# Performance work log

Hardware: AMD Instinct MI355X
Metric: run time of the kernel (lower is better)

## Reference

```python
import jax, jax.numpy as jnp
import numpy as np

EMBED = 1024
HEADS = 16
HEAD_DIM = EMBED // HEADS
LN_EPS = 1e-5
XNORM_GAMMA = 0.01


def xnorm(x, gamma):
    # x * gamma / ||x||_4 along last dim (keepdim)
    norm4 = jnp.sum(x ** 4, axis=-1, keepdims=True) ** 0.25
    return x * gamma / norm4


def setup_inputs() -> dict:
    key = jax.random.key(0)
    ks = jax.random.split(key, 12)
    B, S = 2, 2048
    sc_hd = 1.0 / np.sqrt(HEAD_DIM)
    sc_e = 1.0 / np.sqrt(EMBED)
    return {
        "value": jax.random.normal(ks[0], (B, S, EMBED), jnp.float32),
        "key": jax.random.normal(ks[1], (B, S, EMBED), jnp.float32),
        "query": jax.random.normal(ks[2], (B, S, EMBED), jnp.float32),
        # per-head projections, torch Linear convention: y = x @ W.T
        "Wq": jax.random.normal(ks[3], (HEAD_DIM, HEAD_DIM), jnp.float32) * sc_hd,
        "Wk": jax.random.normal(ks[4], (HEAD_DIM, HEAD_DIM), jnp.float32) * sc_hd,
        "Wv": jax.random.normal(ks[5], (HEAD_DIM, HEAD_DIM), jnp.float32) * sc_hd,
        "Wo": jax.random.normal(ks[6], (EMBED, EMBED), jnp.float32) * sc_e,
        "bo": jnp.zeros((EMBED,), jnp.float32),
        "ln_w": jnp.ones((EMBED,), jnp.float32),
        "ln_b": jnp.zeros((EMBED,), jnp.float32),
        "Wsq": jax.random.normal(ks[7], (EMBED, EMBED), jnp.float32) * sc_e,
        "bsq": jnp.zeros((EMBED,), jnp.float32),
    }


def reference(value, key, query, Wq, Wk, Wv, Wo, bo, ln_w, ln_b, Wsq, bsq):
    B, S, E = query.shape
    # split heads: [B, S, H, D]
    v = value.reshape(B, S, HEADS, HEAD_DIM)
    k = key.reshape(B, S, HEADS, HEAD_DIM)
    q = query.reshape(B, S, HEADS, HEAD_DIM)
    v = jnp.einsum('nshd,ed->nshe', v, Wv)
    k = jnp.einsum('nshd,ed->nshe', k, Wk)
    q = jnp.einsum('nshd,ed->nshe', q, Wq)
    # energy: [B, H, Sq, Sk]
    energy = jnp.einsum('nqhd,nkhd->nhqk', q, k)
    energy_n = xnorm(energy, XNORM_GAMMA)
    v_n = xnorm(v, XNORM_GAMMA)
    out = jnp.einsum('nhql,nlhd->nqhd', energy_n, v_n).reshape(B, S, E)
    attn = out @ Wo.T + bo
    # LayerNorm(attention + query) over embed dim
    x = attn + query
    mu = jnp.mean(x, axis=-1, keepdims=True)
    var = jnp.mean((x - mu) ** 2, axis=-1, keepdims=True)
    x = (x - mu) / jnp.sqrt(var + LN_EPS) * ln_w + ln_b
    # SE gating: x * sigmoid(Linear(x))
    gate = jax.nn.sigmoid(x @ Wsq.T + bsq)
    return x * gate
```

## Files before the change

### kernel.cpp

```cpp
#include <hip/hip_runtime.h>
#include <stdint.h>

#define B_ 2
#define S_ 2048
#define E_ 1024
#define H_ 16
#define HD_ 64
#define N_ (B_*S_)
#define BH_ (B_*H_)
#define GAMMA 0.01f

typedef __attribute__((ext_vector_type(8))) short bf16x8;
typedef __attribute__((ext_vector_type(4))) float f32x4;
typedef __attribute__((ext_vector_type(2))) float f32x2;
typedef __attribute__((ext_vector_type(16))) float f32x16;
typedef __attribute__((ext_vector_type(4))) unsigned int u32x4;
typedef unsigned short u16;
typedef unsigned int u32;

#define SWZ(row, kb) ((kb) ^ (((row)&7)<<4))

__device__ __forceinline__ u16 f2bf(float f){
  union { float f; u32 u; } v; v.f = f;
  return (u16)((v.u + 0x7FFFu + ((v.u>>16)&1u)) >> 16);
}

__device__ __forceinline__ float bf2f(u16 u){
  union { u32 u; float f; } v; v.u = ((u32)u)<<16; return v.f;
}

__device__ __forceinline__ u32 cvt_pk_bf16(float lo, float hi){
  u32 r; asm("v_cvt_pk_bf16_f32 %0, %1, %2" : "=v"(r) : "v"(lo), "v"(hi)); return r;
}

__device__ __forceinline__ uint4 pack8(float4 a, float4 b){
  uint4 r;
  r.x = cvt_pk_bf16(a.x, a.y);
  r.y = cvt_pk_bf16(a.z, a.w);
  r.z = cvt_pk_bf16(b.x, b.y);
  r.w = cvt_pk_bf16(b.z, b.w);
  return r;
}

__device__ __forceinline__ bf16x8 ldfrag(const unsigned char* base, int row, int kbyte){
  return *reinterpret_cast<const bf16x8*>(base + row*128 + SWZ(row, kbyte));
}
__device__ __forceinline__ bf16x8 ldfragV(const unsigned char* base, int row, int col){
  return *reinterpret_cast<const bf16x8*>(base + row*256 + (col ^ ((row&15)<<4)));
}

__device__ __forceinline__ void gl_lds16(const void* g, void* l){
  __builtin_amdgcn_global_load_lds(
      (const __attribute__((address_space(1))) unsigned int*)g,
      (__attribute__((address_space(3))) unsigned int*)l, 16, 0, 0);
}

__device__ __forceinline__ void proj_mfma(const unsigned char* X, const unsigned char* W,
                                          int wid, int l15, int g4, f32x4 acc[4])
{
  f32x4 z = {0.f,0.f,0.f,0.f};
  acc[0]=z; acc[1]=z; acc[2]=z; acc[3]=z;
  #pragma unroll
  for (int kk=0;kk<2;++kk){
    int kbyte = kk*64 + g4*16;
    bf16x8 a = ldfrag(X, wid*16 + l15, kbyte);
    #pragma unroll
    for (int t=0;t<4;++t){
      bf16x8 w = ldfrag(W, t*16 + l15, kbyte);
      acc[t] = __builtin_amdgcn_mfma_f32_16x16x32_bf16(a, w, acc[t], 0, 0, 0);
    }
  }
}

__global__ __launch_bounds__(256) void k_proj(
    const float* __restrict__ qin, const float* __restrict__ kin, const float* __restrict__ vin,
    const float* __restrict__ Wq, const float* __restrict__ Wk, const float* __restrict__ Wv,
    u16* __restrict__ qp, u16* __restrict__ kp, u16* __restrict__ vnT,
    const float* __restrict__ Wo, const float* __restrict__ Wsq,
    u16* __restrict__ wo16, u16* __restrict__ wsq16)
{
  __shared__ alignas(16) unsigned char sm[49152];
  if (blockIdx.y >= H_){
    int cblk = (blockIdx.y - H_)*64 + blockIdx.x;
    int n4 = (E_*E_)/4;
    for (int i = cblk*256 + threadIdx.x; i < 2*n4; i += 128*256){
      const float4* src; ushort4* dst; int j;
      if (i < n4){ src=(const float4*)Wo;  dst=(ushort4*)wo16;  j=i; }
      else       { src=(const float4*)Wsq; dst=(ushort4*)wsq16; j=i-n4; }
      float4 v = src[j];
      ushort4 p; p.x=f2bf(v.x); p.y=f2bf(v.y); p.z=f2bf(v.z); p.w=f2bf(v.w);
      dst[j] = p;
    }
    return;
  }
  const int XQ=0, XK=8192, XV=16384, WQS=24576, WKS=32768, WVS=40960;
  int tid = threadIdx.x, lane = tid&63, wid = tid>>6;
  int l15 = lane&15, g4 = lane>>4;
  int tb = blockIdx.x*64;
  int h  = blockIdx.y;
  int b  = tb >> 11;
  int sbase = tb & 2047;
  int bh = b*H_ + h;

  {
    int rl = tid>>2;
    int d0 = (tid&3)*16;
    const float* xs[3] = { qin, kin, vin };
    const float* wsrc[3] = { Wq, Wk, Wv };
    const int xoff[3] = {XQ,XK,XV}, woff[3] = {WQS,WKS,WVS};
    #pragma unroll
    for (int m3=0;m3<3;++m3){
      const float4* gx = reinterpret_cast<const float4*>(xs[m3] + (size_t)(tb+rl)*E_ + h*HD_ + d0);
      float4 a=gx[0], bb=gx[1], c=gx[2], d=gx[3];
      *(uint4*)(sm + xoff[m3] + rl*128 + SWZ(rl, d0*2))    = pack8(a,bb);
      *(uint4*)(sm + xoff[m3] + rl*128 + SWZ(rl, d0*2+16)) = pack8(c,d);
      const float4* gw = reinterpret_cast<const float4*>(wsrc[m3] + rl*64 + d0);
      float4 e=gw[0], f=gw[1], g2=gw[2], h2=gw[3];
      *(uint4*)(sm + woff[m3] + rl*128 + SWZ(rl, d0*2))    = pack8(e,f);
      *(uint4*)(sm + woff[m3] + rl*128 + SWZ(rl, d0*2+16)) = pack8(g2,h2);
    }
  }
  __syncthreads();

  f32x4 qacc[4], kacc[4], vacc[4];
  proj_mfma(sm+XQ, sm+WQS, wid, l15, g4, qacc);
  proj_mfma(sm+XK, sm+WKS, wid, l15, g4, kacc);
  proj_mfma(sm+XV, sm+WVS, wid, l15, g4, vacc);

  {
    float p4r[4] = {0.f,0.f,0.f,0.f};
    #pragma unroll
    for (int t=0;t<4;++t)
      #pragma unroll
      for (int r=0;r<4;++r){ float e = vacc[t][r]; float e2 = e*e; p4r[r] += e2*e2; }
    #pragma unroll
    for (int r=0;r<4;++r){
      float p = p4r[r];
      p += __shfl_xor(p,1); p += __shfl_xor(p,2); p += __shfl_xor(p,4); p += __shfl_xor(p,8);
      p4r[r] = GAMMA / sqrtf(sqrtf(p));
    }
    #pragma unroll
    for (int t=0;t<4;++t)
      #pragma unroll
      for (int r=0;r<4;++r) vacc[t][r] *= p4r[r];
  }

  __syncthreads();

  #pragma unroll
  for (int t=0;t<4;++t){
    int dd = t*16 + l15;
    #pragma unroll
    for (int r=0;r<4;++r){
      int tokl = wid*16 + g4*4 + r;
      *(u16*)(sm + XQ + tokl*128 + SWZ(tokl, dd*2)) = f2bf(qacc[t][r]);
      *(u16*)(sm + XK + tokl*128 + SWZ(tokl, dd*2)) = f2bf(kacc[t][r]);
    }
    #pragma unroll
    for (int r=0;r<4;r+=2){
      int tokl = wid*16 + g4*4 + r;
      *(u32*)(sm + XV + dd*128 + SWZ(dd, tokl*2)) = cvt_pk_bf16(vacc[t][r], vacc[t][r+1]);
    }
  }
  __syncthreads();

  {
    int rl = tid>>2; int c2 = tid&3;
    uint4 q0 = *(const uint4*)(sm + XQ + rl*128 + SWZ(rl, c2*32));
    uint4 q1 = *(const uint4*)(sm + XQ + rl*128 + SWZ(rl, c2*32+16));
    size_t qg = ((size_t)bh*S_ + sbase + rl)*HD_ + c2*16;
    *(uint4*)(qp + qg)     = q0;
    *(uint4*)(qp + qg + 8) = q1;
    uint4 k0 = *(const uint4*)(sm + XK + rl*128 + SWZ(rl, c2*32));
    uint4 k1 = *(const uint4*)(sm + XK + rl*128 + SWZ(rl, c2*32+16));
    *(uint4*)(kp + qg)     = k0;
    *(uint4*)(kp + qg + 8) = k1;
    uint4 v0 = *(const uint4*)(sm + XV + rl*128 + SWZ(rl, c2*32));
    uint4 v1 = *(const uint4*)(sm + XV + rl*128 + SWZ(rl, c2*32+16));
    size_t vg = ((size_t)bh*HD_ + rl)*S_ + sbase + c2*16;
    *(uint4*)(vnT + vg)     = v0;
    *(uint4*)(vnT + vg + 8) = v1;
  }
}

__global__ __launch_bounds__(256, 2) void k_attn(
    const u16* __restrict__ qp, const u16* __restrict__ kp,
    const u16* __restrict__ vnT, u16* __restrict__ ao)
{
  __shared__ alignas(128) unsigned char sm[81920];
  char* smc = (char*)sm;
  int tid = threadIdx.x, lane = tid&63, wv = tid>>6;
  int l31 = lane&31, hi = lane>>5;
  int qi = wv>>1, kj = wv&1;
  int L = blockIdx.x;
  int xcd = L&7, iw = L>>3;
  int bh = xcd*4 + (iw>>4);
  int qx = iw&15;
  int qb = qx*128;
  int b = bh>>4, h = bh&15;
  const u16* Kb = kp  + (size_t)bh*S_*HD_;
  const u16* Vb = vnT + (size_t)bh*HD_*S_;
  const u16* Qb = qp  + (size_t)bh*S_*HD_;
  int q0 = qb + qi*64;

  bf16x8 qf[2][4];
  #pragma unroll
  for (int f=0;f<2;++f)
    #pragma unroll
    for (int kk=0;kk<4;++kk)
      qf[f][kk] = *reinterpret_cast<const bf16x8*>(Qb + (size_t)(q0 + f*32 + l31)*HD_ + kk*16 + hi*8);

  f32x16 z16 = {};
  f32x16 o[2][2];
  #pragma unroll
  for (int f=0;f<2;++f){ o[f][0] = z16; o[f][1] = z16; }
  f32x2 p4a[2] = {{0.f,0.f},{0.f,0.f}};
  f32x2 p4b[2] = {{0.f,0.f},{0.f,0.f}};

  const char* kSrcC[4]; const char* vSrcC[4];
  #pragma unroll
  for (int c=0;c<4;++c){
    int rk = wv*32 + c*8 + (lane>>3);
    int ck = ((lane&7)*16) ^ ((rk&7)<<4);
    kSrcC[c] = (const char*)Kb + (size_t)rk*128 + ck;
    int rv = wv*16 + c*4 + (lane>>4);
    int cv = ((lane&15)*16) ^ ((rv&15)<<4);
    vSrcC[c] = (const char*)Vb + (size_t)rv*4096 + cv;
  }

  auto STAGE_K = [&](int bsel, int kt){
    char* db = smc + bsel*16384 + wv*4096;
    #pragma unroll
    for (int c=0;c<4;++c) gl_lds16(kSrcC[c] + (size_t)kt*16384, db + c*1024);
  };
  auto STAGE_V = [&](int bsel, int kt){
    char* db = smc + 49152 + bsel*16384 + wv*4096;
    #pragma unroll
    for (int c=0;c<4;++c) gl_lds16(vSrcC[c] + (size_t)kt*256, db + c*1024);
  };

  auto PACK = [&](const f32x16& e, u32 (&w)[4][2], f32x2& pa){
    #pragma unroll
    for (int j=0;j<8;++j){
      const int g=j>>1, i=j&1;
      float a = e[4*g+2*i], c = e[4*g+2*i+1];
      f32x2 pr = {a, c};
      f32x2 e2;
      asm("v_pk_mul_f32 %0, %1, %1" : "=v"(e2) : "v"(pr));
      asm("v_pk_fma_f32 %0, %1, %1, %0" : "+v"(pa) : "v"(e2));
      w[g][i] = cvt_pk_bf16(a, c);
    }
  };
  auto AFRAG = [&](u32 (&w)[4][2], int s) -> bf16x8 {
    u32 a0 = w[2*s][0], b0 = w[2*s+1][0];
    u32 a1 = w[2*s][1], b1 = w[2*s+1][1];
    asm("v_permlane32_swap_b32 %0, %1" : "+v"(a0), "+v"(b0));
    asm("v_permlane32_swap_b32 %0, %1" : "+v"(a1), "+v"(b1));
    u32x4 fw = {a0, a1, b0, b1};
    return __builtin_bit_cast(bf16x8, fw);
  };

  auto QK = [&](const unsigned char* K_, int s2, f32x16& E0, f32x16& E1){
    bf16x8 ka[4];
    #pragma unroll
    for (int kk=0;kk<4;++kk) ka[kk] = ldfrag(K_, kj*64 + s2*32 + l31, kk*32 + hi*16);
    E0 = z16; E1 = z16;
    __builtin_amdgcn_s_setprio(1);
    #pragma unroll
    for (int kk=0;kk<4;++kk){
      E0 = __builtin_amdgcn_mfma_f32_32x32x16_bf16(ka[kk], qf[0][kk], E0, 0,0,0);
      E1 = __builtin_amdgcn_mfma_f32_32x32x16_bf16(ka[kk], qf[1][kk], E1, 0,0,0);
    }
    __builtin_amdgcn_s_setprio(0);
  };

  auto PVF = [&](const unsigned char* V_, int s2, u32 (&w0)[4][2], u32 (&w1)[4][2]){
    bf16x8 vb[2][2];
    #pragma unroll
    for (int s=0;s<2;++s){
      vb[s][0] = ldfragV(V_, l31,    kj*128 + s2*64 + s*32 + hi*16);
      vb[s][1] = ldfragV(V_, 32+l31, kj*128 + s2*64 + s*32 + hi*16);
    }
    __builtin_amdgcn_s_setprio(1);
    #pragma unroll
    for (int s=0;s<2;++s){
      bf16x8 ef0 = AFRAG(w0, s);
      bf16x8 ef1 = AFRAG(w1, s);
      o[0][0] = __builtin_amdgcn_mfma_f32_32x32x16_bf16(ef0, vb[s][0], o[0][0], 0,0,0);
      o[0][1] = __builtin_amdgcn_mfma_f32_32x32x16_bf16(ef0, vb[s][1], o[0][1], 0,0,0);
      o[1][0] = __builtin_amdgcn_mfma_f32_32x32x16_bf16(ef1, vb[s][0], o[1][0], 0,0,0);
      o[1][1] = __builtin_amdgcn_mfma_f32_32x32x16_bf16(ef1, vb[s][1], o[1][1], 0,0,0);
    }
    __builtin_amdgcn_s_setprio(0);
  };

  const int NT = S_/128;
  STAGE_K(0, 0); STAGE_V(0, 0); STAGE_K(1, 1);

  f32x16 eA0, eA1, eB0, eB1;
  u32 wA0[4][2], wA1[4][2], wB0[4][2], wB1[4][2];

  #pragma unroll 1
  for (int t=0; t<NT; ++t){
    if (t < NT-1) { asm volatile("s_waitcnt vmcnt(4)" ::: "memory"); }
    else          { asm volatile("s_waitcnt vmcnt(0)" ::: "memory"); }
    __builtin_amdgcn_s_barrier();
    asm volatile("" ::: "memory");
    if (t+1 < NT) STAGE_V((t+1)&1, t+1);
    if (t+2 < NT) STAGE_K((t+2)%3, t+2);

    const unsigned char* K_ = sm + (t%3)*16384;
    const unsigned char* V_ = sm + 49152 + (t&1)*16384;

    QK(K_, 0, eA0, eA1);
    QK(K_, 1, eB0, eB1);
    PACK(eA0, wA0, p4a[0]);
    PACK(eA1, wA1, p4a[1]);
    PVF(V_, 0, wA0, wA1);
    PACK(eB0, wB0, p4b[0]);
    PACK(eB1, wB1, p4b[1]);
    PVF(V_, 1, wB0, wB1);
  }

  float p4f[2];
  #pragma unroll
  for (int f=0;f<2;++f) p4f[f] = p4a[f].x + p4a[f].y + p4b[f].x + p4b[f].y;

  __syncthreads();
  float* red  = (float*)smc;
  float* redp = (float*)(smc + 32768);
  if (kj==1){
    #pragma unroll
    for (int f=0;f<2;++f){
      #pragma unroll
      for (int ds=0;ds<2;++ds){
        float* dst = red + ((((qi*2+f)*2+ds)*64 + lane)*16);
        #pragma unroll
        for (int r4=0;r4<4;++r4)
          *(float4*)(dst + r4*4) = make_float4(o[f][ds][r4*4],o[f][ds][r4*4+1],o[f][ds][r4*4+2],o[f][ds][r4*4+3]);
      }
      redp[(qi*2+f)*64 + lane] = p4f[f];
    }
  }
  __syncthreads();
  if (kj==0){
    #pragma unroll
    for (int f=0;f<2;++f){
      #pragma unroll
      for (int ds=0;ds<2;++ds){
        const float* srcp = red + ((((qi*2+f)*2+ds)*64 + lane)*16);
        #pragma unroll
        for (int r4=0;r4<4;++r4){
          float4 t = *(const float4*)(srcp + r4*4);
          o[f][ds][r4*4]+=t.x; o[f][ds][r4*4+1]+=t.y; o[f][ds][r4*4+2]+=t.z; o[f][ds][r4*4+3]+=t.w;
        }
      }
      p4f[f] += redp[(qi*2+f)*64 + lane];
      p4f[f] += __shfl_xor(p4f[f], 32);
    }
    float sc0 = GAMMA * rsqrtf(sqrtf(p4f[0]));
    float sc1 = GAMMA * rsqrtf(sqrtf(p4f[1]));
    #pragma unroll
    for (int f=0;f<2;++f){
      #pragma unroll
      for (int r=0;r<16;++r){
        int qrow = (r&3) + 8*(r>>2) + 4*hi;
        float scr = __shfl(f==0 ? sc0 : sc1, qrow);
        size_t n = (size_t)b*S_ + q0 + f*32 + qrow;
        u16* dst = ao + n*E_ + h*HD_;
        dst[l31]    = f2bf(o[f][0][r] * scr);
        dst[32+l31] = f2bf(o[f][1][r] * scr);
      }
    }
  }
}

template<int MODE>
__global__ __launch_bounds__(256, 2) void k_gemm(
    const u16* __restrict__ A, const u16* __restrict__ Bw,
    const float* __restrict__ bias, const float* __restrict__ auxf,
    const u16* __restrict__ aux16, float* __restrict__ out32, u16* __restrict__ out16)
{
  __shared__ alignas(128) unsigned char sm[65536];
  char* smc = (char*)sm;
  int tid = threadIdx.x, lane = tid&63, wv = tid>>6;
  int l31 = lane&31, hi = lane>>5;
  int wr = wv>>1, wc = wv&1;
  int LL = (blockIdx.x & 7)*32 + (blockIdx.x >> 3);
  int mt = LL >> 3, nt = LL & 7;
  int m0 = mt*128, n0 = nt*128;

  const char* aS[4]; const char* bS[4];
  #pragma unroll
  for (int c=0;c<4;++c){
    int off = wv*4096 + c*1024 + lane*16;
    int r = off>>7, cl = off&127;
    int cs = cl ^ ((r&7)<<4);
    aS[c] = (const char*)A  + ((size_t)(m0+r)*E_)*2 + cs;
    bS[c] = (const char*)Bw + ((size_t)(n0+r)*E_)*2 + cs;
  }

  auto STAGE = [&](int bsel, int t){
    char* db = smc + bsel*32768 + wv*4096;
    size_t kb2 = (size_t)t*128;
    #pragma unroll
    for (int c=0;c<4;++c) gl_lds16(aS[c] + kb2, db + c*1024);
    #pragma unroll
    for (int c=0;c<4;++c) gl_lds16(bS[c] + kb2, db + 16384 + c*1024);
  };

  f32x16 acc[2][2] = {{{}, {}}, {{}, {}}};

  const int NK = E_/64;
  STAGE(0, 0); STAGE(1, 1);

  #pragma unroll 1
  for (int t=0; t<NK; ++t){
    if (t < NK-1) { asm volatile("s_waitcnt vmcnt(8)" ::: "memory"); }
    else          { asm volatile("s_waitcnt vmcnt(0)" ::: "memory"); }
    __builtin_amdgcn_s_barrier();
    asm volatile("" ::: "memory");

    const unsigned char* Ap_ = sm + (t&1)*32768;
    const unsigned char* Bp_ = Ap_ + 16384;
    #pragma unroll
    for (int kk=0;kk<4;++kk){
      int kbyte = kk*32 + hi*16;
      bf16x8 a0 = ldfrag(Ap_, wr*64 + l31,      kbyte);
      bf16x8 a1 = ldfrag(Ap_, wr*64 + 32 + l31, kbyte);
      bf16x8 b0 = ldfrag(Bp_, wc*64 + l31,      kbyte);
      bf16x8 b1 = ldfrag(Bp_, wc*64 + 32 + l31, kbyte);
      __builtin_amdgcn_s_setprio(1);
      acc[0][0] = __builtin_amdgcn_mfma_f32_32x32x16_bf16(a0, b0, acc[0][0], 0,0,0);
      acc[0][1] = __builtin_amdgcn_mfma_f32_32x32x16_bf16(a0, b1, acc[0][1], 0,0,0);
      acc[1][0] = __builtin_amdgcn_mfma_f32_32x32x16_bf16(a1, b0, acc[1][0], 0,0,0);
      acc[1][1] = __builtin_amdgcn_mfma_f32_32x32x16_bf16(a1, b1, acc[1][1], 0,0,0);
      __builtin_amdgcn_s_setprio(0);
    }

    asm volatile("" ::: "memory");
    __builtin_amdgcn_s_barrier();
    asm volatile("" ::: "memory");
    if (t+2 < NK) STAGE(t&1, t+2);
  }

  #pragma unroll
  for (int cg=0;cg<2;++cg){
    int col = n0 + wc*64 + cg*32 + l31;
    float bi = bias[col];
    #pragma unroll
    for (int rg=0;rg<2;++rg)
      #pragma unroll
      for (int r=0;r<16;++r){
        int mrow = m0 + wr*64 + rg*32 + (r&3) + 8*(r>>2) + 4*hi;
        size_t idx = (size_t)mrow*E_ + col;
        float v = acc[rg][cg][r] + bi;
        if (MODE == 0){
          out16[idx] = f2bf(v + auxf[idx]);
        } else {
          float gg = 1.f/(1.f + __expf(-v));
          out32[idx] = bf2f(aux16[idx]) * gg;
        }
      }
  }
}

__global__ __launch_bounds__(256) void k_ln(
    const u16* __restrict__ xin, const float* __restrict__ lnw, const float* __restrict__ lnb,
    u16* __restrict__ xout)
{
  __shared__ float red[8];
  __shared__ float stats[2];
  int row = blockIdx.x, tid = threadIdx.x;
  ushort4 xr = reinterpret_cast<const ushort4*>(xin + (size_t)row*E_)[tid];
  float x0 = bf2f(xr.x), x1 = bf2f(xr.y), x2 = bf2f(xr.z), x3 = bf2f(xr.w);
  float s  = x0 + x1 + x2 + x3;
  float s2 = x0*x0 + x1*x1 + x2*x2 + x3*x3;
  #pragma unroll
  for (int m=1;m<64;m<<=1){ s += __shfl_xor(s,m); s2 += __shfl_xor(s2,m); }
  if ((tid&63)==0){ red[tid>>6] = s; red[4+(tid>>6)] = s2; }
  __syncthreads();
  if (tid==0){
    float ts  = red[0]+red[1]+red[2]+red[3];
    float ts2 = red[4]+red[5]+red[6]+red[7];
    float mu  = ts * (1.f/E_);
    float var = ts2 * (1.f/E_) - mu*mu;
    stats[0] = mu; stats[1] = rsqrtf(var + 1e-5f);
  }
  __syncthreads();
  float mu = stats[0], rstd = stats[1];
  float4 w  = reinterpret_cast<const float4*>(lnw)[tid];
  float4 bb = reinterpret_cast<const float4*>(lnb)[tid];
  ushort4 p;
  p.x = f2bf((x0-mu)*rstd*w.x + bb.x);
  p.y = f2bf((x1-mu)*rstd*w.y + bb.y);
  p.z = f2bf((x2-mu)*rstd*w.z + bb.z);
  p.w = f2bf((x3-mu)*rstd*w.w + bb.w);
  reinterpret_cast<ushort4*>(xout + (size_t)row*E_)[tid] = p;
}

extern "C" void kernel_launch(void* const* d_in, const int* in_sizes, int n_in,
                              void* d_out, int out_size, void* d_ws, size_t ws_size,
                              hipStream_t stream)
{
  const float* value = (const float*)d_in[0];
  const float* key   = (const float*)d_in[1];
  const float* query = (const float*)d_in[2];
  const float* Wq    = (const float*)d_in[3];
  const float* Wk    = (const float*)d_in[4];
  const float* Wv    = (const float*)d_in[5];
  const float* Wo    = (const float*)d_in[6];
  const float* bo    = (const float*)d_in[7];
  const float* lnw   = (const float*)d_in[8];
  const float* lnb   = (const float*)d_in[9];
  const float* Wsq   = (const float*)d_in[10];
  const float* bsq   = (const float*)d_in[11];
  float* out = (float*)d_out;

  char* ws = (char*)d_ws;
  const size_t MB = 1ull<<20;
  u16*   qp     = (u16*)(ws + 0*MB);
  u16*   kp     = (u16*)(ws + 8*MB);
  u16*   vnT    = (u16*)(ws + 16*MB);
  u16*   ao     = (u16*)(ws + 24*MB);
  u16*   xres16 = (u16*)(ws + 8*MB);
  u16*   x16    = (u16*)(ws + 16*MB);
  u16*   wo16   = (u16*)(ws + 48*MB);
  u16*   wsq16  = (u16*)(ws + 50*MB);

  k_proj<<<dim3(N_/64, H_+2), 256, 0, stream>>>(query, key, value, Wq, Wk, Wv,
                                                qp, kp, vnT, Wo, Wsq, wo16, wsq16);
  k_attn<<<512, 256, 0, stream>>>(qp, kp, vnT, ao);
  k_gemm<0><<<256, 256, 0, stream>>>(ao, wo16, bo, query, (const u16*)nullptr, (float*)nullptr, xres16);
  k_ln  <<<N_, 256, 0, stream>>>(xres16, lnw, lnb, x16);
  k_gemm<1><<<256, 256, 0, stream>>>(x16, wsq16, bsq, (const float*)nullptr, x16, out, (u16*)nullptr);
}
```

Before: 104.5 us.

## Reassociate attention as Q·(KᵀV) with a separate per-head KᵀV kernel

There is no softmax, and the row-wise 4-norm scale of the energy matrix can be applied after the product. The change therefore computes M = Kᵀ·V_n once per head (64x64) in a new kernel and produces each output row as (q·M) scaled by the energy norm. The attention kernel now only needs the energy pass to accumulate sum(e^4) per query row, and it drops the P·V MFMAs, the V staging and the bf16 packing of the energy. The cost is an extra transposed-K write in the projection kernel and an extra small launch, plus a different rounding order.

```diff
diff --git a/kernel.cpp b/kernel.cpp
--- a/kernel.cpp
+++ b/kernel.cpp
@@ -14,7 +14,6 @@
 typedef __attribute__((ext_vector_type(4))) float f32x4;
 typedef __attribute__((ext_vector_type(2))) float f32x2;
 typedef __attribute__((ext_vector_type(16))) float f32x16;
-typedef __attribute__((ext_vector_type(4))) unsigned int u32x4;
 typedef unsigned short u16;
 typedef unsigned int u32;
 
@@ -45,9 +44,6 @@
 __device__ __forceinline__ bf16x8 ldfrag(const unsigned char* base, int row, int kbyte){
   return *reinterpret_cast<const bf16x8*>(base + row*128 + SWZ(row, kbyte));
 }
-__device__ __forceinline__ bf16x8 ldfragV(const unsigned char* base, int row, int col){
-  return *reinterpret_cast<const bf16x8*>(base + row*256 + (col ^ ((row&15)<<4)));
-}
 
 __device__ __forceinline__ void gl_lds16(const void* g, void* l){
   __builtin_amdgcn_global_load_lds(
@@ -75,7 +71,7 @@
 __global__ __launch_bounds__(256) void k_proj(
     const float* __restrict__ qin, const float* __restrict__ kin, const float* __restrict__ vin,
     const float* __restrict__ Wq, const float* __restrict__ Wk, const float* __restrict__ Wv,
-    u16* __restrict__ qp, u16* __restrict__ kp, u16* __restrict__ vnT,
+    u16* __restrict__ qp, u16* __restrict__ kp, u16* __restrict__ kpT, u16* __restrict__ vnT,
     const float* __restrict__ Wo, const float* __restrict__ Wsq,
     u16* __restrict__ wo16, u16* __restrict__ wsq16)
 {
@@ -159,7 +155,8 @@
     #pragma unroll
     for (int r=0;r<4;r+=2){
       int tokl = wid*16 + g4*4 + r;
-      *(u32*)(sm + XV + dd*128 + SWZ(dd, tokl*2)) = cvt_pk_bf16(vacc[t][r], vacc[t][r+1]);
+      *(u32*)(sm + XV  + dd*128 + SWZ(dd, tokl*2)) = cvt_pk_bf16(vacc[t][r], vacc[t][r+1]);
+      *(u32*)(sm + WQS + dd*128 + SWZ(dd, tokl*2)) = cvt_pk_bf16(kacc[t][r], kacc[t][r+1]);
     }
   }
   __syncthreads();
@@ -175,19 +172,111 @@
     uint4 k1 = *(const uint4*)(sm + XK + rl*128 + SWZ(rl, c2*32+16));
     *(uint4*)(kp + qg)     = k0;
     *(uint4*)(kp + qg + 8) = k1;
+    size_t vg = ((size_t)bh*HD_ + rl)*S_ + sbase + c2*16;
     uint4 v0 = *(const uint4*)(sm + XV + rl*128 + SWZ(rl, c2*32));
     uint4 v1 = *(const uint4*)(sm + XV + rl*128 + SWZ(rl, c2*32+16));
-    size_t vg = ((size_t)bh*HD_ + rl)*S_ + sbase + c2*16;
     *(uint4*)(vnT + vg)     = v0;
     *(uint4*)(vnT + vg + 8) = v1;
+    uint4 t0 = *(const uint4*)(sm + WQS + rl*128 + SWZ(rl, c2*32));
+    uint4 t1 = *(const uint4*)(sm + WQS + rl*128 + SWZ(rl, c2*32+16));
+    *(uint4*)(kpT + vg)     = t0;
+    *(uint4*)(kpT + vg + 8) = t1;
+  }
+}
+
+__global__ __launch_bounds__(256) void k_kv(
+    const u16* __restrict__ kpT, const u16* __restrict__ vnT, u16* __restrict__ MT)
+{
+  __shared__ alignas(128) unsigned char sm[32768];
+  char* smc = (char*)sm;
+  int tid = threadIdx.x, lane = tid&63, wv = tid>>6;
+  int l31 = lane&31, hi = lane>>5;
+  int bh = blockIdx.x;
+  const u16* kt = kpT + (size_t)bh*HD_*S_;
+  const u16* vt = vnT + (size_t)bh*HD_*S_;
+
+  f32x16 acc[2][2] = {{{}, {}}, {{}, {}}};
+  int sbase = wv*512 + hi*8;
+
+  #pragma unroll 2
+  for (int it=0; it<32; ++it){
+    int so = sbase + it*16;
+    bf16x8 ka0 = *reinterpret_cast<const bf16x8*>(kt + (size_t)l31*S_      + so);
+    bf16x8 ka1 = *reinterpret_cast<const bf16x8*>(kt + (size_t)(32+l31)*S_ + so);
+    bf16x8 vb0 = *reinterpret_cast<const bf16x8*>(vt + (size_t)l31*S_      + so);
+    bf16x8 vb1 = *reinterpret_cast<const bf16x8*>(vt + (size_t)(32+l31)*S_ + so);
+    acc[0][0] = __builtin_amdgcn_mfma_f32_32x32x16_bf16(ka0, vb0, acc[0][0], 0,0,0);
+    acc[0][1] = __builtin_amdgcn_mfma_f32_32x32x16_bf16(ka1, vb0, acc[0][1], 0,0,0);
+    acc[1][0] = __builtin_amdgcn_mfma_f32_32x32x16_bf16(ka0, vb1, acc[1][0], 0,0,0);
+    acc[1][1] = __builtin_amdgcn_mfma_f32_32x32x16_bf16(ka1, vb1, acc[1][1], 0,0,0);
+  }
+
+  auto wrAcc = [&](int sl){
+    float* base = (float*)(smc + sl*16384);
+    #pragma unroll
+    for (int eh=0;eh<2;++eh)
+      #pragma unroll
+      for (int dh=0;dh<2;++dh){
+        float* dst = base + (((eh*2+dh)*64 + lane)*16);
+        #pragma unroll
+        for (int r4=0;r4<4;++r4)
+          *(float4*)(dst + r4*4) = make_float4(acc[eh][dh][r4*4],acc[eh][dh][r4*4+1],
+                                               acc[eh][dh][r4*4+2],acc[eh][dh][r4*4+3]);
+      }
+  };
+  auto addAcc = [&](int sl){
+    const float* base = (const float*)(smc + sl*16384);
+    #pragma unroll
+    for (int eh=0;eh<2;++eh)
+      #pragma unroll
+      for (int dh=0;dh<2;++dh){
+        const float* srcp = base + (((eh*2+dh)*64 + lane)*16);
+        #pragma unroll
+        for (int r4=0;r4<4;++r4){
+          float4 t = *(const float4*)(srcp + r4*4);
+          acc[eh][dh][r4*4]+=t.x; acc[eh][dh][r4*4+1]+=t.y;
+          acc[eh][dh][r4*4+2]+=t.z; acc[eh][dh][r4*4+3]+=t.w;
+        }
+      }
+  };
+
+  if (wv==1) wrAcc(0);
+  if (wv==3) wrAcc(1);
+  __syncthreads();
+  if (wv==0) addAcc(0);
+  if (wv==2) addAcc(1);
+  __syncthreads();
+  if (wv==2) wrAcc(0);
+  __syncthreads();
+  if (wv==0) addAcc(0);
+  __syncthreads();
+  if (wv==0){
+    #pragma unroll
+    for (int eh=0;eh<2;++eh)
+      #pragma unroll
+      for (int dh=0;dh<2;++dh)
+        #pragma unroll
+        for (int r=0;r<16;r+=2){
+          int e = eh*32 + l31;
+          int d = dh*32 + (r&3) + 8*(r>>2) + 4*hi;
+          *(u32*)(smc + e*128 + SWZ(e, d*2)) = cvt_pk_bf16(acc[eh][dh][r], acc[eh][dh][r+1]);
+        }
+  }
+  __syncthreads();
+  if (wv==0){
+    u16* dst = MT + (size_t)bh*4096 + lane*64;
+    #pragma unroll
+    for (int c=0;c<8;++c)
+      *(uint4*)(dst + c*8) = *(const uint4*)(smc + lane*128 + SWZ(lane, c*16));
   }
 }
 
 __global__ __launch_bounds__(256, 2) void k_attn(
     const u16* __restrict__ qp, const u16* __restrict__ kp,
-    const u16* __restrict__ vnT, u16* __restrict__ ao)
-{
-  __shared__ alignas(128) unsigned char sm[81920];
+    const u16* __restrict__ MT, u16* __restrict__ ao)
+{
+  __shared__ alignas(128) unsigned char sm[49152];
+  __shared__ float px[256];
   char* smc = (char*)sm;
   int tid = threadIdx.x, lane = tid&63, wv = tid>>6;
   int l31 = lane&31, hi = lane>>5;
@@ -198,9 +287,8 @@
   int qx = iw&15;
   int qb = qx*128;
   int b = bh>>4, h = bh&15;
-  const u16* Kb = kp  + (size_t)bh*S_*HD_;
-  const u16* Vb = vnT + (size_t)bh*HD_*S_;
-  const u16* Qb = qp  + (size_t)bh*S_*HD_;
+  const u16* Kb = kp + (size_t)bh*S_*HD_;
+  const u16* Qb = qp + (size_t)bh*S_*HD_;
   int q0 = qb + qi*64;
 
   bf16x8 qf[2][4];
@@ -211,21 +299,15 @@
       qf[f][kk] = *reinterpret_cast<const bf16x8*>(Qb + (size_t)(q0 + f*32 + l31)*HD_ + kk*16 + hi*8);
 
   f32x16 z16 = {};
-  f32x16 o[2][2];
-  #pragma unroll
-  for (int f=0;f<2;++f){ o[f][0] = z16; o[f][1] = z16; }
   f32x2 p4a[2] = {{0.f,0.f},{0.f,0.f}};
   f32x2 p4b[2] = {{0.f,0.f},{0.f,0.f}};
 
-  const char* kSrcC[4]; const char* vSrcC[4];
+  const char* kSrcC[4];
   #pragma unroll
   for (int c=0;c<4;++c){
     int rk = wv*32 + c*8 + (lane>>3);
     int ck = ((lane&7)*16) ^ ((rk&7)<<4);
     kSrcC[c] = (const char*)Kb + (size_t)rk*128 + ck;
-    int rv = wv*16 + c*4 + (lane>>4);
-    int cv = ((lane&15)*16) ^ ((rv&15)<<4);
-    vSrcC[c] = (const char*)Vb + (size_t)rv*4096 + cv;
   }
 
   auto STAGE_K = [&](int bsel, int kt){
@@ -233,31 +315,15 @@
     #pragma unroll
     for (int c=0;c<4;++c) gl_lds16(kSrcC[c] + (size_t)kt*16384, db + c*1024);
   };
-  auto STAGE_V = [&](int bsel, int kt){
-    char* db = smc + 49152 + bsel*16384 + wv*4096;
-    #pragma unroll
-    for (int c=0;c<4;++c) gl_lds16(vSrcC[c] + (size_t)kt*256, db + c*1024);
-  };
-
-  auto PACK = [&](const f32x16& e, u32 (&w)[4][2], f32x2& pa){
+
+  auto P4ACC = [&](const f32x16& e, f32x2& pa){
     #pragma unroll
     for (int j=0;j<8;++j){
-      const int g=j>>1, i=j&1;
-      float a = e[4*g+2*i], c = e[4*g+2*i+1];
-      f32x2 pr = {a, c};
+      f32x2 pr = {e[2*j], e[2*j+1]};
       f32x2 e2;
       asm("v_pk_mul_f32 %0, %1, %1" : "=v"(e2) : "v"(pr));
       asm("v_pk_fma_f32 %0, %1, %1, %0" : "+v"(pa) : "v"(e2));
-      w[g][i] = cvt_pk_bf16(a, c);
-    }
-  };
-  auto AFRAG = [&](u32 (&w)[4][2], int s) -> bf16x8 {
-    u32 a0 = w[2*s][0], b0 = w[2*s+1][0];
-    u32 a1 = w[2*s][1], b1 = w[2*s+1][1];
-    asm("v_permlane32_swap_b32 %0, %1" : "+v"(a0), "+v"(b0));
-    asm("v_permlane32_swap_b32 %0, %1" : "+v"(a1), "+v"(b1));
-    u32x4 fw = {a0, a1, b0, b1};
-    return __builtin_bit_cast(bf16x8, fw);
+    }
   };
 
   auto QK = [&](const unsigned char* K_, int s2, f32x16& E0, f32x16& E1){
@@ -274,31 +340,10 @@
     __builtin_amdgcn_s_setprio(0);
   };
 
-  auto PVF = [&](const unsigned char* V_, int s2, u32 (&w0)[4][2], u32 (&w1)[4][2]){
-    bf16x8 vb[2][2];
-    #pragma unroll
-    for (int s=0;s<2;++s){
-      vb[s][0] = ldfragV(V_, l31,    kj*128 + s2*64 + s*32 + hi*16);
-      vb[s][1] = ldfragV(V_, 32+l31, kj*128 + s2*64 + s*32 + hi*16);
-    }
-    __builtin_amdgcn_s_setprio(1);
-    #pragma unroll
-    for (int s=0;s<2;++s){
-      bf16x8 ef0 = AFRAG(w0, s);
-      bf16x8 ef1 = AFRAG(w1, s);
-      o[0][0] = __builtin_amdgcn_mfma_f32_32x32x16_bf16(ef0, vb[s][0], o[0][0], 0,0,0);
-      o[0][1] = __builtin_amdgcn_mfma_f32_32x32x16_bf16(ef0, vb[s][1], o[0][1], 0,0,0);
-      o[1][0] = __builtin_amdgcn_mfma_f32_32x32x16_bf16(ef1, vb[s][0], o[1][0], 0,0,0);
-      o[1][1] = __builtin_amdgcn_mfma_f32_32x32x16_bf16(ef1, vb[s][1], o[1][1], 0,0,0);
-    }
-    __builtin_amdgcn_s_setprio(0);
-  };
-
   const int NT = S_/128;
-  STAGE_K(0, 0); STAGE_V(0, 0); STAGE_K(1, 1);
+  STAGE_K(0, 0); STAGE_K(1, 1);
 
   f32x16 eA0, eA1, eB0, eB1;
-  u32 wA0[4][2], wA1[4][2], wB0[4][2], wB1[4][2];
 
   #pragma unroll 1
   for (int t=0; t<NT; ++t){
@@ -306,72 +351,62 @@
     else          { asm volatile("s_waitcnt vmcnt(0)" ::: "memory"); }
     __builtin_amdgcn_s_barrier();
     asm volatile("" ::: "memory");
-    if (t+1 < NT) STAGE_V((t+1)&1, t+1);
     if (t+2 < NT) STAGE_K((t+2)%3, t+2);
 
     const unsigned char* K_ = sm + (t%3)*16384;
-    const unsigned char* V_ = sm + 49152 + (t&1)*16384;
-
     QK(K_, 0, eA0, eA1);
     QK(K_, 1, eB0, eB1);
-    PACK(eA0, wA0, p4a[0]);
-    PACK(eA1, wA1, p4a[1]);
-    PVF(V_, 0, wA0, wA1);
-    PACK(eB0, wB0, p4b[0]);
-    PACK(eB1, wB1, p4b[1]);
-    PVF(V_, 1, wB0, wB1);
+    P4ACC(eA0, p4a[0]);
+    P4ACC(eA1, p4a[1]);
+    P4ACC(eB0, p4b[0]);
+    P4ACC(eB1, p4b[1]);
   }
 
   float p4f[2];
   #pragma unroll
-  for (int f=0;f<2;++f) p4f[f] = p4a[f].x + p4a[f].y + p4b[f].x + p4b[f].y;
-
-  __syncthreads();
-  float* red  = (float*)smc;
-  float* redp = (float*)(smc + 32768);
-  if (kj==1){
-    #pragma unroll
-    for (int f=0;f<2;++f){
-      #pragma unroll
-      for (int ds=0;ds<2;++ds){
-        float* dst = red + ((((qi*2+f)*2+ds)*64 + lane)*16);
-        #pragma unroll
-        for (int r4=0;r4<4;++r4)
-          *(float4*)(dst + r4*4) = make_float4(o[f][ds][r4*4],o[f][ds][r4*4+1],o[f][ds][r4*4+2],o[f][ds][r4*4+3]);
-      }
-      redp[(qi*2+f)*64 + lane] = p4f[f];
-    }
-  }
-  __syncthreads();
-  if (kj==0){
-    #pragma unroll
-    for (int f=0;f<2;++f){
-      #pragma unroll
-      for (int ds=0;ds<2;++ds){
-        const float* srcp = red + ((((qi*2+f)*2+ds)*64 + lane)*16);
-        #pragma unroll
-        for (int r4=0;r4<4;++r4){
-          float4 t = *(const float4*)(srcp + r4*4);
-          o[f][ds][r4*4]+=t.x; o[f][ds][r4*4+1]+=t.y; o[f][ds][r4*4+2]+=t.z; o[f][ds][r4*4+3]+=t.w;
-        }
-      }
-      p4f[f] += redp[(qi*2+f)*64 + lane];
-      p4f[f] += __shfl_xor(p4f[f], 32);
-    }
-    float sc0 = GAMMA * rsqrtf(sqrtf(p4f[0]));
-    float sc1 = GAMMA * rsqrtf(sqrtf(p4f[1]));
-    #pragma unroll
-    for (int f=0;f<2;++f){
-      #pragma unroll
-      for (int r=0;r<16;++r){
-        int qrow = (r&3) + 8*(r>>2) + 4*hi;
-        float scr = __shfl(f==0 ? sc0 : sc1, qrow);
-        size_t n = (size_t)b*S_ + q0 + f*32 + qrow;
-        u16* dst = ao + n*E_ + h*HD_;
-        dst[l31]    = f2bf(o[f][0][r] * scr);
-        dst[32+l31] = f2bf(o[f][1][r] * scr);
-      }
-    }
+  for (int f=0;f<2;++f){
+    p4f[f] = p4a[f].x + p4a[f].y + p4b[f].x + p4b[f].y;
+    p4f[f] += __shfl_xor(p4f[f], 32);
+  }
+  __syncthreads();
+  if (hi==0){
+    px[((qi*2+0)*2+kj)*32 + l31] = p4f[0];
+    px[((qi*2+1)*2+kj)*32 + l31] = p4f[1];
+  }
+  __syncthreads();
+  #pragma unroll
+  for (int f=0;f<2;++f) p4f[f] += px[((qi*2+f)*2+(1-kj))*32 + l31];
+  float sc0 = GAMMA * rsqrtf(sqrtf(p4f[0]));
+  float sc1 = GAMMA * rsqrtf(sqrtf(p4f[1]));
+
+  const u16* mtb = MT + (size_t)bh*4096;
+  bf16x8 mtf[4];
+  #pragma unroll
+  for (int kk=0;kk<4;++kk)
+    mtf[kk] = *reinterpret_cast<const bf16x8*>(mtb + (kj*32 + l31)*64 + kk*16 + hi*8);
+  f32x16 oA0 = z16, oA1 = z16;
+  #pragma unroll
+  for (int kk=0;kk<4;++kk){
+    oA0 = __builtin_amdgcn_mfma_f32_32x32x16_bf16(mtf[kk], qf[0][kk], oA0, 0,0,0);
+    oA1 = __builtin_amdgcn_mfma_f32_32x32x16_bf16(mtf[kk], qf[1][kk], oA1, 0,0,0);
+  }
+
+  __syncthreads();
+  #pragma unroll
+  for (int r=0;r<16;r+=2){
+    int e = kj*32 + (r&3) + 8*(r>>2) + 4*hi;
+    int ql0 = qi*64 + l31;
+    *(u32*)(smc + ql0*128 + SWZ(ql0, e*2))         = cvt_pk_bf16(oA0[r]*sc0, oA0[r+1]*sc0);
+    int ql1 = qi*64 + 32 + l31;
+    *(u32*)(smc + ql1*128 + SWZ(ql1, e*2))         = cvt_pk_bf16(oA1[r]*sc1, oA1[r+1]*sc1);
+  }
+  __syncthreads();
+  {
+    int row = tid>>1, eh = tid&1;
+    u16* dst = ao + ((size_t)b*S_ + qb + row)*E_ + h*HD_ + eh*32;
+    #pragma unroll
+    for (int c=0;c<4;++c)
+      *(uint4*)(dst + c*8) = *(const uint4*)(smc + row*128 + SWZ(row, eh*64 + c*16));
   }
 }
 
@@ -522,15 +557,18 @@
   u16*   qp     = (u16*)(ws + 0*MB);
   u16*   kp     = (u16*)(ws + 8*MB);
   u16*   vnT    = (u16*)(ws + 16*MB);
-  u16*   ao     = (u16*)(ws + 24*MB);
+  u16*   kpT    = (u16*)(ws + 24*MB);
+  u16*   ao     = (u16*)(ws + 32*MB);
+  u16*   mtw    = (u16*)(ws + 44*MB);
   u16*   xres16 = (u16*)(ws + 8*MB);
   u16*   x16    = (u16*)(ws + 16*MB);
   u16*   wo16   = (u16*)(ws + 48*MB);
   u16*   wsq16  = (u16*)(ws + 50*MB);
 
   k_proj<<<dim3(N_/64, H_+2), 256, 0, stream>>>(query, key, value, Wq, Wk, Wv,
-                                                qp, kp, vnT, Wo, Wsq, wo16, wsq16);
-  k_attn<<<512, 256, 0, stream>>>(qp, kp, vnT, ao);
+                                                qp, kp, kpT, vnT, Wo, Wsq, wo16, wsq16);
+  k_kv  <<<BH_, 256, 0, stream>>>(kpT, vnT, mtw);
+  k_attn<<<512, 256, 0, stream>>>(qp, kp, mtw, ao);
   k_gemm<0><<<256, 256, 0, stream>>>(ao, wo16, bo, query, (const u16*)nullptr, (float*)nullptr, xres16);
   k_ln  <<<N_, 256, 0, stream>>>(xres16, lnw, lnb, x16);
   k_gemm<1><<<256, 256, 0, stream>>>(x16, wsq16, bsq, (const float*)nullptr, x16, out, (u16*)nullptr);
```

New measurement: 111.8 us. +7.0%, slower.
